# Kernel optimization log

Measured on AMD Instinct MI355X. Metric: run time of the kernel, lower is better.

Reference implementation:

```python
import jax, jax.numpy as jnp
import numpy as np

DIM = 1024          # n_embd
NUM_EXPERTS = 8
TOP_K = 2
HIDDEN = 4 * DIM // TOP_K   # expert_hidden_dim = 2048
BS, SLEN = 1, 2048


def setup_inputs() -> dict:
    key = jax.random.key(0)
    k0, k1, k2, k3 = jax.random.split(key, 4)
    x = jax.random.normal(k0, (BS, SLEN, DIM), dtype=jnp.float32)
    gate_w = jax.random.normal(k1, (NUM_EXPERTS, DIM), dtype=jnp.float32) * 0.02
    w_up = jax.random.normal(k2, (NUM_EXPERTS, HIDDEN, DIM), dtype=jnp.float32) * 0.02
    w_down = jax.random.normal(k3, (NUM_EXPERTS, DIM, HIDDEN), dtype=jnp.float32) * 0.02
    expert_bias = jnp.zeros((NUM_EXPERTS,), dtype=jnp.float32)
    return {"x": x, "gate_w": gate_w, "w_up": w_up, "w_down": w_down,
            "expert_bias": expert_bias}


def _moe(x, gate_w, w_up, w_down, expert_bias):
    bs, slen, dim = x.shape
    xf = x.reshape(-1, dim)                       # (T, D)
    # Sigmoid router (scores in fp32, bias only affects selection, not weights)
    scores = jax.nn.sigmoid(xf @ gate_w.T)        # (T, E)
    biased = scores + expert_bias
    _, sel = jax.lax.top_k(biased, TOP_K)         # (T, K) expert ids, distinct per token
    top_scores = jnp.take_along_axis(scores, sel, axis=-1)  # (T, K)

    # Scatter/gather dispatch + grouped GEMM is mathematically equivalent to:
    #   out[t] = sum_k W_down[e_tk] @ relu(W_up[e_tk] @ (s_tk * x[t]))^2
    # Loop over the small fixed expert set via lax.scan; unassigned tokens
    # contribute exactly zero (relu(0)^2 = 0), honoring the routing sparsity.
    def body(acc, ew):
        e, wu, wd = ew
        # combined routing weight for this expert per token (at most one slot)
        w_t = jnp.sum(jnp.where(sel == e, top_scores, 0.0), axis=-1)  # (T,)
        xe = xf * w_t[:, None]                    # (T, D), zero for non-routed
        h = jnp.square(jax.nn.relu(xe @ wu.T))    # (T, H)  relu(x)^2 activation
        return acc + h @ wd.T, None

    out0 = jnp.zeros_like(xf)
    out, _ = jax.lax.scan(body, out0, (jnp.arange(NUM_EXPERTS), w_up, w_down))
    return out.reshape(bs, slen, dim)


def reference(x, gate_w, w_up, w_down, expert_bias):
    return _moe(x, gate_w, w_up, w_down, expert_bias)
```

## Files before the change

### kernel.cpp

```cpp
#include <hip/hip_runtime.h>
#include <cstdint>
#include <cstddef>

#define T_TOK 2048
#define DMODEL 1024
#define NEXP 8
#define HID 2048
#define DUMP_ID 4096

typedef __bf16 bf16x8 __attribute__((ext_vector_type(8)));
typedef float f32x4 __attribute__((ext_vector_type(4)));
typedef unsigned short u16;
typedef u16 u16x8 __attribute__((ext_vector_type(8)));

__device__ __forceinline__ u16 f2bf(float f) {
    union { float f; unsigned int u; } v; v.f = f;
    unsigned int u = v.u;
    unsigned int r = (u + 0x7FFFu + ((u >> 16) & 1u)) >> 16;
    return (u16)r;
}

__device__ __forceinline__ void gl2lds16(const void* g, void* l) {
    __builtin_amdgcn_global_load_lds(
        (const __attribute__((address_space(1))) void*)g,
        (__attribute__((address_space(3))) void*)l,
        16, 0, 0);
}

__global__ void init_k(int* __restrict__ counts, int* __restrict__ list,
                       unsigned short* __restrict__ xb_dump_row) {
    int i = blockIdx.x * blockDim.x + threadIdx.x;
    if (i < NEXP) counts[i] = 0;
    if (i < NEXP * T_TOK) list[i] = DUMP_ID;
    if (i < DMODEL) xb_dump_row[i] = 0;
}

__global__ __launch_bounds__(64) void router_k(
    const float* __restrict__ x, const float* __restrict__ gw,
    const float* __restrict__ bias, unsigned short* __restrict__ xb,
    int* __restrict__ counts, int* __restrict__ list, float* __restrict__ w2) {
    const int t = blockIdx.x;
    const int lane = threadIdx.x;
    const float* xr = x + (size_t)t * DMODEL;
    float acc[NEXP];
#pragma unroll
    for (int e = 0; e < NEXP; ++e) acc[e] = 0.f;
#pragma unroll
    for (int j = 0; j < DMODEL / 64; ++j) {
        int i = lane + j * 64;
        float xv = xr[i];
        xb[(size_t)t * DMODEL + i] = f2bf(xv);
#pragma unroll
        for (int e = 0; e < NEXP; ++e) acc[e] += xv * gw[e * DMODEL + i];
    }
#pragma unroll
    for (int e = 0; e < NEXP; ++e)
        for (int off = 32; off > 0; off >>= 1) acc[e] += __shfl_xor(acc[e], off, 64);
    if (lane == 0) {
        float sc[NEXP], bi[NEXP];
#pragma unroll
        for (int e = 0; e < NEXP; ++e) {
            sc[e] = 1.f / (1.f + expf(-acc[e]));
            bi[e] = sc[e] + bias[e];
        }
        int e0 = 0;
        for (int e = 1; e < NEXP; ++e) if (bi[e] > bi[e0]) e0 = e;
        int e1 = -1;
        for (int e = 0; e < NEXP; ++e) {
            if (e == e0) continue;
            if (e1 < 0 || bi[e] > bi[e1]) e1 = e;
        }
        int s0 = atomicAdd(&counts[e0], 1);
        list[e0 * T_TOK + s0] = 2 * t;
        int s1 = atomicAdd(&counts[e1], 1);
        list[e1 * T_TOK + s1] = 2 * t + 1;
        w2[2 * t]     = sc[e0] * sc[e0];
        w2[2 * t + 1] = sc[e1] * sc[e1];
    }
}

__global__ void convert_w(const float4* __restrict__ wu, const float4* __restrict__ wd,
                          u16x8* __restrict__ wub, u16x8* __restrict__ wdb, int n8) {
    int i = blockIdx.x * blockDim.x + threadIdx.x;
    const float4* src; u16x8* dst; int idx;
    if (i < n8) { src = wu; dst = wub; idx = i; }
    else        { src = wd; dst = wdb; idx = i - n8; }
    float4 a = src[2 * idx], b = src[2 * idx + 1];
    u16x8 o = {f2bf(a.x), f2bf(a.y), f2bf(a.z), f2bf(a.w),
               f2bf(b.x), f2bf(b.y), f2bf(b.z), f2bf(b.w)};
    dst[idx] = o;
}

template <int MODE>
__global__ __launch_bounds__(256, 2) void moe_gemm(
    const u16* __restrict__ Asrc, const int* __restrict__ list,
    const int* __restrict__ counts, const u16* __restrict__ Ball,
    const float* __restrict__ w2, u16* __restrict__ Hout,
    float* __restrict__ Cout) {
    constexpr int K   = (MODE == 0) ? DMODEL : HID;
    constexpr int N   = (MODE == 0) ? HID : DMODEL;
    constexpr int NKT = K / 64;
    constexpr int NTN = N / 128;
    constexpr int LOGNTN = (MODE == 0) ? 4 : 3;

    const int b = blockIdx.x;
    const int e = b & 7;
    const int rest = b >> 3;
    const int m0 = (rest >> LOGNTN) * 128;
    if (m0 >= counts[e]) return;
    const int n0 = (rest & (NTN - 1)) * 128;

    const int tid = threadIdx.x;
    const int lane = tid & 63;
    const int w = tid >> 6;

    __shared__ u16 As[128 * 64];
    __shared__ u16 Bs[128 * 64];

    const int* mylist = list + e * T_TOK + m0;
    const u16* B = Ball + (size_t)e * HID * DMODEL;

    const u16* ap[4];
    const u16* bp[4];
#pragma unroll
    for (int it = 0; it < 4; ++it) {
        int row = it * 32 + (tid >> 3);
        int gs = (tid & 7) ^ (row & 7);
        int id = mylist[row];
        int arow = (MODE == 0) ? (id >> 1) : id;
        ap[it] = Asrc + (size_t)arow * K + gs * 8;
        bp[it] = B + (size_t)(n0 + row) * K + gs * 8;
    }

    const int wm = (w >> 1) * 64;
    const int wn = (w & 1) * 64;
    const int quad = lane >> 4;
    const int lrow = lane & 15;

    f32x4 acc[4][4];
#pragma unroll
    for (int i = 0; i < 4; ++i)
#pragma unroll
        for (int j = 0; j < 4; ++j) acc[i][j] = f32x4{0.f, 0.f, 0.f, 0.f};

    for (int kt = 0; kt < NKT; ++kt) {
#pragma unroll
        for (int it = 0; it < 4; ++it)
            gl2lds16(ap[it] + kt * 64, &As[(it * 256 + w * 64) * 8]);
#pragma unroll
        for (int it = 0; it < 4; ++it)
            gl2lds16(bp[it] + kt * 64, &Bs[(it * 256 + w * 64) * 8]);
        __syncthreads();
#pragma unroll
        for (int s = 0; s < 2; ++s) {
            const int q = s * 4 + quad;
            bf16x8 af[4], bfr[4];
#pragma unroll
            for (int i = 0; i < 4; ++i) {
                int ra = wm + i * 16 + lrow;
                int rb = wn + i * 16 + lrow;
                af[i]  = *(const bf16x8*)&As[ra * 64 + (q ^ (ra & 7)) * 8];
                bfr[i] = *(const bf16x8*)&Bs[rb * 64 + (q ^ (rb & 7)) * 8];
            }
#pragma unroll
            for (int i = 0; i < 4; ++i)
#pragma unroll
                for (int j = 0; j < 4; ++j)
                    acc[i][j] = __builtin_amdgcn_mfma_f32_16x16x32_bf16(
                        af[i], bfr[j], acc[i][j], 0, 0, 0);
        }
        __syncthreads();
    }

#pragma unroll
    for (int i = 0; i < 4; ++i) {
        int mbase = wm + i * 16 + (lane >> 4) * 4;
        int ids[4];
        float ww[4];
#pragma unroll
        for (int r = 0; r < 4; ++r) {
            ids[r] = mylist[mbase + r];
            if (MODE == 0) ww[r] = w2[ids[r]];
        }
#pragma unroll
        for (int j = 0; j < 4; ++j) {
            int n = n0 + wn + j * 16 + (lane & 15);
#pragma unroll
            for (int r = 0; r < 4; ++r) {
                float v = acc[i][j][r];
                if (MODE == 0) {
                    v = (v > 0.f) ? v * v * ww[r] : 0.f;
                    Hout[(size_t)ids[r] * HID + n] = f2bf(v);
                } else {
                    Cout[(size_t)ids[r] * DMODEL + n] = v;
                }
            }
        }
    }
}

__global__ void combine_k(const float4* __restrict__ c, float4* __restrict__ out) {
    int i = blockIdx.x * blockDim.x + threadIdx.x;
    if (i >= T_TOK * (DMODEL / 4)) return;
    int t = i >> 8;
    int d = i & 255;
    float4 a = c[(size_t)(2 * t) * (DMODEL / 4) + d];
    float4 b = c[(size_t)(2 * t + 1) * (DMODEL / 4) + d];
    float4 o;
    o.x = a.x + b.x; o.y = a.y + b.y; o.z = a.z + b.z; o.w = a.w + b.w;
    out[i] = o;
}

extern "C" void kernel_launch(void* const* d_in, const int* in_sizes, int n_in,
                              void* d_out, int out_size, void* d_ws, size_t ws_size,
                              hipStream_t stream) {
    const float* x      = (const float*)d_in[0];
    const float* gate_w = (const float*)d_in[1];
    const float* w_up   = (const float*)d_in[2];
    const float* w_down = (const float*)d_in[3];
    const float* bias   = (const float*)d_in[4];
    float* out = (float*)d_out;

    char* p = (char*)d_ws;
    int* counts = (int*)p;              p += 256;
    int* list   = (int*)p;              p += NEXP * T_TOK * 4;
    float* w2   = (float*)p;            p += 4104 * 4;
    u16* xb  = (u16*)p;  p += (size_t)(T_TOK + 1) * DMODEL * 2;
    u16* wub = (u16*)p;  p += (size_t)NEXP * HID * DMODEL * 2;
    u16* wdb = (u16*)p;  p += (size_t)NEXP * HID * DMODEL * 2;
    u16* h   = (u16*)p;  p += (size_t)(2 * T_TOK + 1) * HID * 2;
    float* c = (float*)p; p += (size_t)(2 * T_TOK + 1) * DMODEL * 4;

    init_k<<<64, 256, 0, stream>>>(counts, list, xb + (size_t)T_TOK * DMODEL);

    router_k<<<T_TOK, 64, 0, stream>>>(x, gate_w, bias, xb, counts, list, w2);

    {
        int n8 = NEXP * HID * DMODEL / 8;
        convert_w<<<(2 * n8) / 256, 256, 0, stream>>>(
            (const float4*)w_up, (const float4*)w_down,
            (u16x8*)wub, (u16x8*)wdb, n8);
    }

    moe_gemm<0><<<16 * (HID / 128) * NEXP, 256, 0, stream>>>(
        xb, list, counts, wub, w2, h, nullptr);

    moe_gemm<1><<<16 * (DMODEL / 128) * NEXP, 256, 0, stream>>>(
        h, list, counts, wdb, w2, nullptr, c);

    combine_k<<<(T_TOK * (DMODEL / 4) + 255) / 256, 256, 0, stream>>>(
        (const float4*)c, (float4*)out);
}
```

Baseline: 299.5 us.

## Fuse preprocessing kernels, build expert lists by ballot, atomically accumulate down-proj output

Merges the weight conversion, init and router into one launch, with each router wave now handling two tokens. Expert lists are built deterministically with a per-expert ballot/prefix-scan kernel instead of global atomics. The down-projection GEMM atomically adds straight into the zeroed output, which removes the combine kernel and the fp32 intermediate buffer. This cuts launches and memory traffic at the cost of float atomics, which make the summation order nondeterministic, plus a memset.

```diff
diff --git a/kernel.cpp b/kernel.cpp
--- a/kernel.cpp
+++ b/kernel.cpp
@@ -7,6 +7,7 @@
 #define NEXP 8
 #define HID 2048
 #define DUMP_ID 4096
+#define NB_CONV 8192
 
 typedef __bf16 bf16x8 __attribute__((ext_vector_type(8)));
 typedef float f32x4 __attribute__((ext_vector_type(4)));
@@ -27,68 +28,123 @@
         16, 0, 0);
 }
 
-__global__ void init_k(int* __restrict__ counts, int* __restrict__ list,
-                       unsigned short* __restrict__ xb_dump_row) {
-    int i = blockIdx.x * blockDim.x + threadIdx.x;
-    if (i < NEXP) counts[i] = 0;
-    if (i < NEXP * T_TOK) list[i] = DUMP_ID;
-    if (i < DMODEL) xb_dump_row[i] = 0;
-}
-
-__global__ __launch_bounds__(64) void router_k(
-    const float* __restrict__ x, const float* __restrict__ gw,
-    const float* __restrict__ bias, unsigned short* __restrict__ xb,
-    int* __restrict__ counts, int* __restrict__ list, float* __restrict__ w2) {
-    const int t = blockIdx.x;
-    const int lane = threadIdx.x;
-    const float* xr = x + (size_t)t * DMODEL;
-    float acc[NEXP];
-#pragma unroll
-    for (int e = 0; e < NEXP; ++e) acc[e] = 0.f;
-#pragma unroll
-    for (int j = 0; j < DMODEL / 64; ++j) {
-        int i = lane + j * 64;
-        float xv = xr[i];
-        xb[(size_t)t * DMODEL + i] = f2bf(xv);
-#pragma unroll
-        for (int e = 0; e < NEXP; ++e) acc[e] += xv * gw[e * DMODEL + i];
+__global__ __launch_bounds__(256) void fused_pre(
+    const float4* __restrict__ wu4, const float4* __restrict__ wd4,
+    ushort4* __restrict__ wub4, ushort4* __restrict__ wdb4,
+    const float4* __restrict__ x4, const float4* __restrict__ gw4,
+    const float* __restrict__ bias, ushort4* __restrict__ xb4,
+    unsigned int* __restrict__ selpack, float* __restrict__ w2,
+    unsigned int* __restrict__ xb_dump_row_u32) {
+    const int b = blockIdx.x;
+    const int tid = threadIdx.x;
+
+    if (b < NB_CONV) {
+        const int n4u = NEXP * HID * DMODEL / 4;
+        int i0 = b * 256 + tid;
+#pragma unroll
+        for (int c = 0; c < 4; ++c) {
+            int idx = i0 + c * (NB_CONV * 256);
+            float4 f = (idx < n4u) ? wu4[idx] : wd4[idx - n4u];
+            ushort4 o;
+            o.x = f2bf(f.x); o.y = f2bf(f.y); o.z = f2bf(f.z); o.w = f2bf(f.w);
+            if (idx < n4u) wub4[idx] = o; else wdb4[idx - n4u] = o;
+        }
+        return;
+    }
+    if (b == NB_CONV + 256) {
+        if (tid < DMODEL / 2) xb_dump_row_u32[tid] = 0;
+        return;
+    }
+    const int rb = b - NB_CONV;
+    const int wv = tid >> 6;
+    const int lane = tid & 63;
+    const int pair = rb * 4 + wv;
+    const int t0 = 2 * pair, t1 = t0 + 1;
+
+    float acc0[NEXP], acc1[NEXP];
+#pragma unroll
+    for (int e = 0; e < NEXP; ++e) { acc0[e] = 0.f; acc1[e] = 0.f; }
+#pragma unroll
+    for (int j = 0; j < 4; ++j) {
+        int i4 = lane + j * 64;
+        float4 a0 = x4[t0 * 256 + i4];
+        float4 a1 = x4[t1 * 256 + i4];
+        ushort4 s0, s1;
+        s0.x = f2bf(a0.x); s0.y = f2bf(a0.y); s0.z = f2bf(a0.z); s0.w = f2bf(a0.w);
+        s1.x = f2bf(a1.x); s1.y = f2bf(a1.y); s1.z = f2bf(a1.z); s1.w = f2bf(a1.w);
+        xb4[t0 * 256 + i4] = s0;
+        xb4[t1 * 256 + i4] = s1;
+#pragma unroll
+        for (int e = 0; e < NEXP; ++e) {
+            float4 g = gw4[e * 256 + i4];
+            acc0[e] += a0.x * g.x + a0.y * g.y + a0.z * g.z + a0.w * g.w;
+            acc1[e] += a1.x * g.x + a1.y * g.y + a1.z * g.z + a1.w * g.w;
+        }
     }
 #pragma unroll
     for (int e = 0; e < NEXP; ++e)
-        for (int off = 32; off > 0; off >>= 1) acc[e] += __shfl_xor(acc[e], off, 64);
+        for (int off = 32; off > 0; off >>= 1) {
+            acc0[e] += __shfl_xor(acc0[e], off, 64);
+            acc1[e] += __shfl_xor(acc1[e], off, 64);
+        }
     if (lane == 0) {
-        float sc[NEXP], bi[NEXP];
-#pragma unroll
-        for (int e = 0; e < NEXP; ++e) {
-            sc[e] = 1.f / (1.f + expf(-acc[e]));
-            bi[e] = sc[e] + bias[e];
-        }
-        int e0 = 0;
-        for (int e = 1; e < NEXP; ++e) if (bi[e] > bi[e0]) e0 = e;
-        int e1 = -1;
-        for (int e = 0; e < NEXP; ++e) {
-            if (e == e0) continue;
-            if (e1 < 0 || bi[e] > bi[e1]) e1 = e;
-        }
-        int s0 = atomicAdd(&counts[e0], 1);
-        list[e0 * T_TOK + s0] = 2 * t;
-        int s1 = atomicAdd(&counts[e1], 1);
-        list[e1 * T_TOK + s1] = 2 * t + 1;
-        w2[2 * t]     = sc[e0] * sc[e0];
-        w2[2 * t + 1] = sc[e1] * sc[e1];
-    }
-}
-
-__global__ void convert_w(const float4* __restrict__ wu, const float4* __restrict__ wd,
-                          u16x8* __restrict__ wub, u16x8* __restrict__ wdb, int n8) {
-    int i = blockIdx.x * blockDim.x + threadIdx.x;
-    const float4* src; u16x8* dst; int idx;
-    if (i < n8) { src = wu; dst = wub; idx = i; }
-    else        { src = wd; dst = wdb; idx = i - n8; }
-    float4 a = src[2 * idx], b = src[2 * idx + 1];
-    u16x8 o = {f2bf(a.x), f2bf(a.y), f2bf(a.z), f2bf(a.w),
-               f2bf(b.x), f2bf(b.y), f2bf(b.z), f2bf(b.w)};
-    dst[idx] = o;
+#pragma unroll
+        for (int tt = 0; tt < 2; ++tt) {
+            int t = tt ? t1 : t0;
+            float sc[NEXP], bi[NEXP];
+#pragma unroll
+            for (int e = 0; e < NEXP; ++e) {
+                float a = tt ? acc1[e] : acc0[e];
+                sc[e] = 1.f / (1.f + expf(-a));
+                bi[e] = sc[e] + bias[e];
+            }
+            int e0 = 0;
+            for (int e = 1; e < NEXP; ++e) if (bi[e] > bi[e0]) e0 = e;
+            int e1 = -1;
+            for (int e = 0; e < NEXP; ++e) {
+                if (e == e0) continue;
+                if (e1 < 0 || bi[e] > bi[e1]) e1 = e;
+            }
+            selpack[t] = (unsigned int)e0 | ((unsigned int)e1 << 8);
+            w2[2 * t]     = sc[e0] * sc[e0];
+            w2[2 * t + 1] = sc[e1] * sc[e1];
+        }
+    }
+}
+
+__global__ __launch_bounds__(256) void build_lists(
+    const unsigned int* __restrict__ selpack, int* __restrict__ counts,
+    int* __restrict__ list) {
+    const int e = blockIdx.x;
+    const int tid = threadIdx.x;
+    const int lane = tid & 63;
+    const int wv = tid >> 6;
+    __shared__ int wsum[4];
+    __shared__ int base;
+    if (tid == 0) base = 0;
+    __syncthreads();
+    for (int tb = 0; tb < T_TOK; tb += 256) {
+        int t = tb + tid;
+        unsigned int sp = selpack[t];
+        bool f1 = ((sp >> 8) & 255u) == (unsigned)e;
+        bool f = ((sp & 255u) == (unsigned)e) | f1;
+        int id = 2 * t + (f1 ? 1 : 0);
+        unsigned long long m = __ballot(f);
+        int pos = __popcll(m & ((1ull << lane) - 1ull));
+        if (lane == 0) wsum[wv] = __popcll(m);
+        __syncthreads();
+        int woff = 0;
+#pragma unroll
+        for (int i = 0; i < 4; ++i) if (i < wv) woff += wsum[i];
+        int bse = base;
+        if (f) list[e * T_TOK + bse + woff + pos] = id;
+        __syncthreads();
+        if (tid == 0) base = bse + wsum[0] + wsum[1] + wsum[2] + wsum[3];
+    }
+    __syncthreads();
+    int total = base;
+    if (tid == 0) counts[e] = total;
+    for (int i = total + tid; i < T_TOK; i += 256) list[e * T_TOK + i] = DUMP_ID;
 }
 
 template <int MODE>
@@ -192,23 +248,12 @@
                     v = (v > 0.f) ? v * v * ww[r] : 0.f;
                     Hout[(size_t)ids[r] * HID + n] = f2bf(v);
                 } else {
-                    Cout[(size_t)ids[r] * DMODEL + n] = v;
+                    if (ids[r] != DUMP_ID)
+                        atomicAdd(&Cout[(size_t)(ids[r] >> 1) * DMODEL + n], v);
                 }
             }
         }
     }
-}
-
-__global__ void combine_k(const float4* __restrict__ c, float4* __restrict__ out) {
-    int i = blockIdx.x * blockDim.x + threadIdx.x;
-    if (i >= T_TOK * (DMODEL / 4)) return;
-    int t = i >> 8;
-    int d = i & 255;
-    float4 a = c[(size_t)(2 * t) * (DMODEL / 4) + d];
-    float4 b = c[(size_t)(2 * t + 1) * (DMODEL / 4) + d];
-    float4 o;
-    o.x = a.x + b.x; o.y = a.y + b.y; o.z = a.z + b.z; o.w = a.w + b.w;
-    out[i] = o;
 }
 
 extern "C" void kernel_launch(void* const* d_in, const int* in_sizes, int n_in,
@@ -222,32 +267,29 @@
     float* out = (float*)d_out;
 
     char* p = (char*)d_ws;
-    int* counts = (int*)p;              p += 256;
-    int* list   = (int*)p;              p += NEXP * T_TOK * 4;
-    float* w2   = (float*)p;            p += 4104 * 4;
+    int* counts = (int*)p;                 p += 256;
+    int* list   = (int*)p;                 p += NEXP * T_TOK * 4;
+    float* w2   = (float*)p;               p += 4104 * 4;
+    unsigned int* selpack = (unsigned int*)p;  p += T_TOK * 4;
     u16* xb  = (u16*)p;  p += (size_t)(T_TOK + 1) * DMODEL * 2;
     u16* wub = (u16*)p;  p += (size_t)NEXP * HID * DMODEL * 2;
     u16* wdb = (u16*)p;  p += (size_t)NEXP * HID * DMODEL * 2;
     u16* h   = (u16*)p;  p += (size_t)(2 * T_TOK + 1) * HID * 2;
-    float* c = (float*)p; p += (size_t)(2 * T_TOK + 1) * DMODEL * 4;
-
-    init_k<<<64, 256, 0, stream>>>(counts, list, xb + (size_t)T_TOK * DMODEL);
-
-    router_k<<<T_TOK, 64, 0, stream>>>(x, gate_w, bias, xb, counts, list, w2);
-
-    {
-        int n8 = NEXP * HID * DMODEL / 8;
-        convert_w<<<(2 * n8) / 256, 256, 0, stream>>>(
-            (const float4*)w_up, (const float4*)w_down,
-            (u16x8*)wub, (u16x8*)wdb, n8);
-    }
+
+    hipMemsetAsync(d_out, 0, (size_t)out_size * sizeof(float), stream);
+
+    fused_pre<<<NB_CONV + 256 + 1, 256, 0, stream>>>(
+        (const float4*)w_up, (const float4*)w_down,
+        (ushort4*)wub, (ushort4*)wdb,
+        (const float4*)x, (const float4*)gate_w, bias,
+        (ushort4*)xb, selpack, w2,
+        (unsigned int*)(xb + (size_t)T_TOK * DMODEL));
+
+    build_lists<<<NEXP, 256, 0, stream>>>(selpack, counts, list);
 
     moe_gemm<0><<<16 * (HID / 128) * NEXP, 256, 0, stream>>>(
         xb, list, counts, wub, w2, h, nullptr);
 
     moe_gemm<1><<<16 * (DMODEL / 128) * NEXP, 256, 0, stream>>>(
-        h, list, counts, wdb, w2, nullptr, c);
-
-    combine_k<<<(T_TOK * (DMODEL / 4) + 255) / 256, 256, 0, stream>>>(
-        (const float4*)c, (float4*)out);
-}
+        h, list, counts, wdb, w2, nullptr, out);
+}
```

Result: faster. 264.7 us (-11.6%).
